# Optimization experiments

Measured on AMD Instinct MI355X. Metric: run time of the kernel, lower is better.

Reference implementation:

```python
import jax, jax.numpy as jnp
import numpy as np

BLK = 64      # NF4 quantization blocksize
SUPER = 256   # double-quant blocksize over absmax

# NF4 codebook (bitsandbytes normal-float-4 lookup table)
NF4 = jnp.array([
    -1.0, -0.6961928009986877, -0.5250730514526367, -0.39491748809814453,
    -0.28444138169288635, -0.18477343022823334, -0.09105003625154495, 0.0,
    0.07958029955625534, 0.16093020141124725, 0.24611230194568634,
    0.33791524171829224, 0.44070982933044434, 0.5626170039176941,
    0.7229568362236023, 1.0], dtype=jnp.float32)


def setup_inputs() -> dict:
    key = jax.random.key(0)
    k1, k2, k3, k4, k5, k6 = jax.random.split(key, 6)
    B, S, I, O = 4, 2048, 4096, 4096
    n_blocks = O * I // BLK            # 262144
    n_super = n_blocks // SUPER        # 1024
    return {
        "x": jax.random.normal(k1, (B, S, I), dtype=jnp.float32),
        "w_codes": jax.random.randint(k2, (O, I), 0, 16, dtype=jnp.int32),
        "absmax_codes": jax.random.randint(k3, (n_blocks,), 0, 256, dtype=jnp.int32),
        "absmax_scale": jax.random.uniform(k4, (n_super,), dtype=jnp.float32),
        "absmax_offset": jax.random.uniform(k5, (1,), dtype=jnp.float32),
        "bias": jax.random.normal(k6, (O,), dtype=jnp.float32),
    }


def reference(x, w_codes, absmax_codes, absmax_scale, absmax_offset, bias):
    O, I = w_codes.shape
    # --- double-quant: dequantize 8-bit absmax codes blockwise (SUPER) ---
    # absmax[b] = code/255 * scale[superblock(b)] + offset
    am = absmax_codes.astype(jnp.float32) / 255.0          # [n_blocks]
    am = am.reshape(-1, SUPER) * absmax_scale[:, None] + absmax_offset[0]
    absmax = am.reshape(O, I // BLK)                        # per-64 block scale
    # --- NF4 dequant: lookup-table value * blockwise absmax ---
    w = NF4[w_codes].reshape(O, I // BLK, BLK) * absmax[:, :, None]
    w = w.reshape(O, I)                                     # [O, I] fp32
    # --- GEMM + bias (compute_dtype analog) ---
    return jnp.einsum('bsi,oi->bso', x, w) + bias
```

## Files before the change

kernel.cpp:

```cpp
#include <hip/hip_runtime.h>
#include <cstdint>
#include <cstddef>

#define DIM_M 8192
#define DIM_N 4096
#define DIM_K 4096

#define BLK_M 128
#define BLK_N 128
#define BLK_K 32

typedef __bf16 bf16x8 __attribute__((ext_vector_type(8)));
typedef float floatx16 __attribute__((ext_vector_type(16)));
typedef float fvec4 __attribute__((ext_vector_type(4)));
typedef int   ivec4 __attribute__((ext_vector_type(4)));
typedef unsigned int uvec4 __attribute__((ext_vector_type(4)));

__device__ __constant__ float NF4_TAB[16] = {
    -1.0f, -0.6961928009986877f, -0.5250730514526367f, -0.39491748809814453f,
    -0.28444138169288635f, -0.18477343022823334f, -0.09105003625154495f, 0.0f,
    0.07958029955625534f, 0.16093020141124725f, 0.24611230194568634f,
    0.33791524171829224f, 0.44070982933044434f, 0.5626170039176941f,
    0.7229568362236023f, 1.0f};

__device__ inline unsigned short f2bf(float f) {
    unsigned int u = __builtin_bit_cast(unsigned int, f);
    u += 0x7fffu + ((u >> 16) & 1u);
    return (unsigned short)(u >> 16);
}

__global__ void prep_kernel(const float* __restrict__ x, unsigned short* __restrict__ xb,
                            const int* __restrict__ codes,
                            const int* __restrict__ am_codes,
                            const float* __restrict__ am_scale,
                            const float* __restrict__ am_off,
                            unsigned short* __restrict__ wb,
                            int xcv_blocks) {
    if ((int)blockIdx.x < xcv_blocks) {
        size_t base = ((size_t)blockIdx.x * blockDim.x + threadIdx.x) * 8;
        fvec4 a = __builtin_nontemporal_load((const fvec4*)(x + base));
        fvec4 b = __builtin_nontemporal_load((const fvec4*)(x + base + 4));
        unsigned short r[8];
        r[0] = f2bf(a.x); r[1] = f2bf(a.y); r[2] = f2bf(a.z); r[3] = f2bf(a.w);
        r[4] = f2bf(b.x); r[5] = f2bf(b.y); r[6] = f2bf(b.z); r[7] = f2bf(b.w);
        *(uvec4*)(xb + base) = *(const uvec4*)r;
    } else {
        __shared__ float nf4[16];
        if (threadIdx.x < 16) nf4[threadIdx.x] = NF4_TAB[threadIdx.x];
        __syncthreads();
        size_t base = ((size_t)(blockIdx.x - xcv_blocks) * blockDim.x + threadIdx.x) * 8;
        int blk = (int)(base >> 6);
        float absmax = (float)am_codes[blk] * (1.0f / 255.0f) * am_scale[blk >> 8] + am_off[0];
        ivec4 c0 = __builtin_nontemporal_load((const ivec4*)(codes + base));
        ivec4 c1 = __builtin_nontemporal_load((const ivec4*)(codes + base + 4));
        unsigned short r[8];
        r[0] = f2bf(nf4[c0.x & 15] * absmax);
        r[1] = f2bf(nf4[c0.y & 15] * absmax);
        r[2] = f2bf(nf4[c0.z & 15] * absmax);
        r[3] = f2bf(nf4[c0.w & 15] * absmax);
        r[4] = f2bf(nf4[c1.x & 15] * absmax);
        r[5] = f2bf(nf4[c1.y & 15] * absmax);
        r[6] = f2bf(nf4[c1.z & 15] * absmax);
        r[7] = f2bf(nf4[c1.w & 15] * absmax);
        *(uvec4*)(wb + base) = *(const uvec4*)r;
    }
}

__device__ inline void gld_lds16(const void* g, void* l) {
    __builtin_amdgcn_global_load_lds((__attribute__((address_space(1))) void*)g,
                                     (__attribute__((address_space(3))) void*)l,
                                     16, 0, 0);
}

__global__ __launch_bounds__(256) void gemm_bt(const unsigned short* __restrict__ A,
                                               const unsigned short* __restrict__ B,
                                               const float* __restrict__ bias,
                                               float* __restrict__ C,
                                               int M, int N, int K) {
    __shared__ __attribute__((aligned(16))) unsigned short lA[BLK_M * BLK_K];
    __shared__ __attribute__((aligned(16))) unsigned short lB[BLK_N * BLK_K];
    const int tid = threadIdx.x;
    const int wave = tid >> 6;
    const int lane = tid & 63;

    const int l = blockIdx.y * gridDim.x + blockIdx.x;
    const int bn = (l >> 3) & 31;
    const int bm = ((l >> 8) << 3) + (l & 7);

    const int wm = (wave >> 1) * 64;
    const int wn = (wave & 1) * 64;

    const int er0 = tid >> 2;
    const int cg  = (tid & 3) ^ ((tid >> 3) & 3);
    const unsigned short* gA = A + (size_t)(bm * BLK_M + er0) * K + cg * 8;
    const unsigned short* gB = B + (size_t)(bn * BLK_N + er0) * K + cg * 8;
    unsigned short* lA0 = &lA[tid * 8];
    unsigned short* lA1 = &lA[2048 + tid * 8];
    unsigned short* lB0 = &lB[tid * 8];
    unsigned short* lB1 = &lB[2048 + tid * 8];
    const size_t rstride = (size_t)64 * K;

    floatx16 acc[2][2];
#pragma unroll
    for (int i = 0; i < 2; ++i)
#pragma unroll
        for (int j = 0; j < 2; ++j)
#pragma unroll
            for (int r = 0; r < 16; ++r) acc[i][j][r] = 0.0f;

    const int arow = lane & 31;
    const int half = lane >> 5;
    const int swz = (arow >> 1) & 3;

    for (int k0 = 0; k0 < K; k0 += BLK_K) {
        gld_lds16(gA, lA0);
        gld_lds16(gA + rstride, lA1);
        gld_lds16(gB, lB0);
        gld_lds16(gB + rstride, lB1);
        gA += BLK_K;
        gB += BLK_K;
        __syncthreads();

        bf16x8 af[2][2], bfr[2][2];
#pragma unroll
        for (int s = 0; s < 2; ++s) {
            const int co = (((s << 1) + half) ^ swz) * 8;
#pragma unroll
            for (int i = 0; i < 2; ++i) {
                af[i][s]  = *(const bf16x8*)&lA[(wm + i * 32 + arow) * BLK_K + co];
                bfr[i][s] = *(const bf16x8*)&lB[(wn + i * 32 + arow) * BLK_K + co];
            }
        }
#pragma unroll
        for (int s = 0; s < 2; ++s)
#pragma unroll
            for (int i = 0; i < 2; ++i)
#pragma unroll
                for (int j = 0; j < 2; ++j)
                    acc[i][j] = __builtin_amdgcn_mfma_f32_32x32x16_bf16(af[i][s], bfr[j][s], acc[i][j], 0, 0, 0);
        __syncthreads();
    }

#pragma unroll
    for (int j = 0; j < 2; ++j) {
        int gn = bn * BLK_N + wn + j * 32 + arow;
        float bv = bias[gn];
#pragma unroll
        for (int i = 0; i < 2; ++i) {
            int gm0 = bm * BLK_M + wm + i * 32 + half * 4;
#pragma unroll
            for (int r = 0; r < 16; ++r) {
                int row = (r & 3) + ((r >> 2) << 3);
                __builtin_nontemporal_store(acc[i][j][r] + bv,
                                            C + (size_t)(gm0 + row) * N + gn);
            }
        }
    }
}

extern "C" void kernel_launch(void* const* d_in, const int* in_sizes, int n_in,
                              void* d_out, int out_size, void* d_ws, size_t ws_size,
                              hipStream_t stream) {
    const float* x        = (const float*)d_in[0];
    const int*   w_codes  = (const int*)d_in[1];
    const int*   am_codes = (const int*)d_in[2];
    const float* am_scale = (const float*)d_in[3];
    const float* am_off   = (const float*)d_in[4];
    const float* bias     = (const float*)d_in[5];
    float* out = (float*)d_out;

    const int M = DIM_M, N = DIM_N, K = DIM_K;

    unsigned short* xb = (unsigned short*)d_ws;
    unsigned short* wb = xb + (size_t)M * K;

    {
        int xcv_blocks = (int)(((size_t)M * K) / 8 / 256);
        int wdq_blocks = (int)(((size_t)N * K) / 8 / 256);
        prep_kernel<<<xcv_blocks + wdq_blocks, 256, 0, stream>>>(
            x, xb, w_codes, am_codes, am_scale, am_off, wb, xcv_blocks);
    }
    {
        dim3 grid(N / BLK_N, M / BLK_M);
        gemm_bt<<<grid, 256, 0, stream>>>(xb, wb, bias, out, M, N, K);
    }
}
```

Before: 579.1 us.

## Rewrite GEMM with 256x256 tiles, 4-stage LDS pipeline and 16x16 MFMA

Measured after the change: 509.5 us. -12.0%, faster.

```diff
diff --git a/kernel.cpp b/kernel.cpp
--- a/kernel.cpp
+++ b/kernel.cpp
@@ -6,12 +6,12 @@
 #define DIM_N 4096
 #define DIM_K 4096
 
-#define BLK_M 128
-#define BLK_N 128
-#define BLK_K 32
+#define BM 256
+#define BN 256
+#define BK 32
+#define NT (DIM_K / BK)
 
 typedef __bf16 bf16x8 __attribute__((ext_vector_type(8)));
-typedef float floatx16 __attribute__((ext_vector_type(16)));
 typedef float fvec4 __attribute__((ext_vector_type(4)));
 typedef int   ivec4 __attribute__((ext_vector_type(4)));
 typedef unsigned int uvec4 __attribute__((ext_vector_type(4)));
@@ -72,88 +72,124 @@
                                      16, 0, 0);
 }
 
-__global__ __launch_bounds__(256) void gemm_bt(const unsigned short* __restrict__ A,
-                                               const unsigned short* __restrict__ B,
-                                               const float* __restrict__ bias,
-                                               float* __restrict__ C,
-                                               int M, int N, int K) {
-    __shared__ __attribute__((aligned(16))) unsigned short lA[BLK_M * BLK_K];
-    __shared__ __attribute__((aligned(16))) unsigned short lB[BLK_N * BLK_K];
-    const int tid = threadIdx.x;
+__global__ __launch_bounds__(512, 2) void gemm_bt(const unsigned short* __restrict__ A,
+                                                  const unsigned short* __restrict__ B,
+                                                  const float* __restrict__ bias,
+                                                  float* __restrict__ C,
+                                                  int M, int N, int K) {
+    __shared__ __attribute__((aligned(16))) unsigned short lA[4][BM * BK];
+    __shared__ __attribute__((aligned(16))) unsigned short lB[4][BN * BK];
+
+    const int tid  = threadIdx.x;
     const int wave = tid >> 6;
     const int lane = tid & 63;
 
-    const int l = blockIdx.y * gridDim.x + blockIdx.x;
-    const int bn = (l >> 3) & 31;
-    const int bm = ((l >> 8) << 3) + (l & 7);
-
-    const int wm = (wave >> 1) * 64;
-    const int wn = (wave & 1) * 64;
-
-    const int er0 = tid >> 2;
-    const int cg  = (tid & 3) ^ ((tid >> 3) & 3);
-    const unsigned short* gA = A + (size_t)(bm * BLK_M + er0) * K + cg * 8;
-    const unsigned short* gB = B + (size_t)(bn * BLK_N + er0) * K + cg * 8;
-    unsigned short* lA0 = &lA[tid * 8];
-    unsigned short* lA1 = &lA[2048 + tid * 8];
-    unsigned short* lB0 = &lB[tid * 8];
-    unsigned short* lB1 = &lB[2048 + tid * 8];
-    const size_t rstride = (size_t)64 * K;
-
-    floatx16 acc[2][2];
-#pragma unroll
-    for (int i = 0; i < 2; ++i)
-#pragma unroll
-        for (int j = 0; j < 2; ++j)
-#pragma unroll
-            for (int r = 0; r < 16; ++r) acc[i][j][r] = 0.0f;
-
-    const int arow = lane & 31;
-    const int half = lane >> 5;
-    const int swz = (arow >> 1) & 3;
-
-    for (int k0 = 0; k0 < K; k0 += BLK_K) {
-        gld_lds16(gA, lA0);
-        gld_lds16(gA + rstride, lA1);
-        gld_lds16(gB, lB0);
-        gld_lds16(gB + rstride, lB1);
-        gA += BLK_K;
-        gB += BLK_K;
-        __syncthreads();
-
-        bf16x8 af[2][2], bfr[2][2];
-#pragma unroll
-        for (int s = 0; s < 2; ++s) {
-            const int co = (((s << 1) + half) ^ swz) * 8;
-#pragma unroll
-            for (int i = 0; i < 2; ++i) {
-                af[i][s]  = *(const bf16x8*)&lA[(wm + i * 32 + arow) * BLK_K + co];
-                bfr[i][s] = *(const bf16x8*)&lB[(wn + i * 32 + arow) * BLK_K + co];
-            }
+    const int orig = (int)blockIdx.x;
+    const int xcd = orig & 7;
+    const int idx = orig >> 3;
+    const int bm = ((idx >> 4) << 3) + xcd;
+    const int bn = idx & 15;
+
+    const int wr = wave >> 2;
+    const int wc = wave & 3;
+    const int wm = wr * 128;
+    const int wn = wc * 64;
+
+    const int srow = tid >> 2;
+    const int gch  = (tid & 3) ^ ((tid >> 3) & 3);
+    const unsigned short* sA0 = A + (size_t)(bm * BM + srow) * K + gch * 8;
+    const unsigned short* sA1 = sA0 + (size_t)128 * K;
+    const unsigned short* sB0 = B + (size_t)(bn * BN + srow) * K + gch * 8;
+    const unsigned short* sB1 = sB0 + (size_t)128 * K;
+
+    const int cslot = (lane >> 4) ^ ((lane >> 1) & 3);
+    const int aoff = (wm + (lane & 15)) * BK + cslot * 8;
+    const int boff = (wn + (lane & 15)) * BK + cslot * 8;
+
+    fvec4 acc[8][4];
+#pragma unroll
+    for (int m = 0; m < 8; ++m)
+#pragma unroll
+        for (int n = 0; n < 4; ++n)
+#pragma unroll
+            for (int r = 0; r < 4; ++r) acc[m][n][r] = 0.0f;
+
+#pragma unroll
+    for (int pt = 0; pt < 3; ++pt) {
+        const int kb = pt * BK;
+        gld_lds16(sA0 + kb, &lA[pt][tid * 8]);
+        gld_lds16(sA1 + kb, &lA[pt][(tid + 512) * 8]);
+        gld_lds16(sB0 + kb, &lB[pt][tid * 8]);
+        gld_lds16(sB1 + kb, &lB[pt][(tid + 512) * 8]);
+    }
+    asm volatile("s_waitcnt vmcnt(8)" ::: "memory");
+    __builtin_amdgcn_s_barrier();
+
+    for (int t = 0; t < NT; ++t) {
+        const int b = t & 3;
+        const unsigned short* la = lA[b];
+        const unsigned short* lb = lB[b];
+
+        bf16x8 a0[4], bv[4];
+#pragma unroll
+        for (int m = 0; m < 4; ++m) a0[m] = *(const bf16x8*)(la + aoff + m * 512);
+#pragma unroll
+        for (int n = 0; n < 4; ++n) bv[n] = *(const bf16x8*)(lb + boff + n * 512);
+        if (t + 3 < NT) {
+            const int nb = (t + 3) & 3;
+            const size_t kb = (size_t)(t + 3) * BK;
+            gld_lds16(sA0 + kb, &lA[nb][tid * 8]);
+            gld_lds16(sA1 + kb, &lA[nb][(tid + 512) * 8]);
         }
-#pragma unroll
-        for (int s = 0; s < 2; ++s)
-#pragma unroll
-            for (int i = 0; i < 2; ++i)
-#pragma unroll
-                for (int j = 0; j < 2; ++j)
-                    acc[i][j] = __builtin_amdgcn_mfma_f32_32x32x16_bf16(af[i][s], bfr[j][s], acc[i][j], 0, 0, 0);
-        __syncthreads();
-    }
-
-#pragma unroll
-    for (int j = 0; j < 2; ++j) {
-        int gn = bn * BLK_N + wn + j * 32 + arow;
-        float bv = bias[gn];
-#pragma unroll
-        for (int i = 0; i < 2; ++i) {
-            int gm0 = bm * BLK_M + wm + i * 32 + half * 4;
-#pragma unroll
-            for (int r = 0; r < 16; ++r) {
-                int row = (r & 3) + ((r >> 2) << 3);
-                __builtin_nontemporal_store(acc[i][j][r] + bv,
-                                            C + (size_t)(gm0 + row) * N + gn);
-            }
+        __builtin_amdgcn_s_barrier();
+        asm volatile("s_waitcnt lgkmcnt(0)" ::: "memory");
+        __builtin_amdgcn_sched_barrier(0);
+        __builtin_amdgcn_s_setprio(1);
+#pragma unroll
+        for (int m = 0; m < 4; ++m)
+#pragma unroll
+            for (int n = 0; n < 4; ++n)
+                acc[m][n] = __builtin_amdgcn_mfma_f32_16x16x32_bf16(a0[m], bv[n], acc[m][n], 0, 0, 0);
+        __builtin_amdgcn_s_setprio(0);
+        __builtin_amdgcn_s_barrier();
+
+        bf16x8 a1[4];
+#pragma unroll
+        for (int m = 0; m < 4; ++m) a1[m] = *(const bf16x8*)(la + aoff + (m + 4) * 512);
+        if (t + 3 < NT) {
+            const int nb = (t + 3) & 3;
+            const size_t kb = (size_t)(t + 3) * BK;
+            gld_lds16(sB0 + kb, &lB[nb][tid * 8]);
+            gld_lds16(sB1 + kb, &lB[nb][(tid + 512) * 8]);
+        }
+        __builtin_amdgcn_s_barrier();
+        asm volatile("s_waitcnt lgkmcnt(0)" ::: "memory");
+        __builtin_amdgcn_sched_barrier(0);
+        __builtin_amdgcn_s_setprio(1);
+#pragma unroll
+        for (int m = 0; m < 4; ++m)
+#pragma unroll
+            for (int n = 0; n < 4; ++n)
+                acc[m + 4][n] = __builtin_amdgcn_mfma_f32_16x16x32_bf16(a1[m], bv[n], acc[m + 4][n], 0, 0, 0);
+        __builtin_amdgcn_s_setprio(0);
+
+        if (t < NT - 3)       { asm volatile("s_waitcnt vmcnt(8)" ::: "memory"); }
+        else if (t == NT - 3) { asm volatile("s_waitcnt vmcnt(4)" ::: "memory"); }
+        else if (t == NT - 2) { asm volatile("s_waitcnt vmcnt(0)" ::: "memory"); }
+        if (t < NT - 1) __builtin_amdgcn_s_barrier();
+    }
+
+    const int col0 = bn * BN + wn + (lane & 15);
+    const int row0 = bm * BM + wm + ((lane >> 4) << 2);
+#pragma unroll
+    for (int n = 0; n < 4; ++n) {
+        const float bvs = bias[col0 + n * 16];
+#pragma unroll
+        for (int m = 0; m < 8; ++m) {
+            float* cp = C + (size_t)(row0 + m * 16) * N + col0 + n * 16;
+#pragma unroll
+            for (int r = 0; r < 4; ++r)
+                __builtin_nontemporal_store(acc[m][n][r] + bvs, cp + (size_t)r * N);
         }
     }
 }
@@ -181,7 +217,7 @@
             x, xb, w_codes, am_codes, am_scale, am_off, wb, xcv_blocks);
     }
     {
-        dim3 grid(N / BLK_N, M / BLK_M);
-        gemm_bt<<<grid, 256, 0, stream>>>(xb, wb, bias, out, M, N, K);
-    }
-}
+        dim3 grid((M / BM) * (N / BN));
+        gemm_bt<<<grid, 512, 0, stream>>>(xb, wb, bias, out, M, N, K);
+    }
+}
```
